# Kernel tuning notes

Measured on AMD Instinct MI355X. Metric: run time of the kernel, lower is better.

The kernel has to match this reference:

```python
import jax, jax.numpy as jnp
import numpy as np

# Model dims (match init_kwargs)
D_MODEL = 512
NUM_EXPERTS = 8
TOP_K = 2
FFN_MULT = 2
HIDDEN = FFN_MULT * D_MODEL
BATCH, SEQ = 4, 2048


def setup_inputs() -> dict:
    key = jax.random.key(0)
    k_x, k_g, k_bg, k_w1, k_w3, k_w2 = jax.random.split(key, 6)
    sd = 1.0 / np.sqrt(D_MODEL).astype(np.float32)
    sh = 1.0 / np.sqrt(HIDDEN).astype(np.float32)
    return {
        "x": jax.random.normal(k_x, (BATCH, SEQ, D_MODEL), dtype=jnp.float32),
        # gate: nn.Linear(d_model, num_experts) with bias
        "Wg": jax.random.normal(k_g, (D_MODEL, NUM_EXPERTS), dtype=jnp.float32) * sd,
        "bg": jax.random.normal(k_bg, (NUM_EXPERTS,), dtype=jnp.float32) * 0.01,
        # stacked per-expert SwiGLU FFN params (no bias, LLaMA-style)
        "W1": jax.random.normal(k_w1, (NUM_EXPERTS, D_MODEL, HIDDEN), dtype=jnp.float32) * sd,
        "W3": jax.random.normal(k_w3, (NUM_EXPERTS, D_MODEL, HIDDEN), dtype=jnp.float32) * sd,
        "W2": jax.random.normal(k_w2, (NUM_EXPERTS, HIDDEN, D_MODEL), dtype=jnp.float32) * sh,
    }


def reference(x, Wg, bg, W1, W3, W2):
    B, S, D = x.shape
    E = Wg.shape[1]
    xt = x.reshape(-1, D)                        # [T, D], T = B*S
    T = xt.shape[0]

    # Router: top-k over experts, softmax over the k selected logits
    logits = xt @ Wg + bg                        # [T, E]
    top_vals, top_idx = jax.lax.top_k(logits, TOP_K)  # [T, K]
    top_probs = jax.nn.softmax(top_vals, axis=-1)     # [T, K]

    # Dense per-(token, expert) combine weight; zero where expert not selected.
    # top-k indices are distinct per token so scatter-add == scatter-set.
    gate_w = jnp.zeros((T, E), dtype=xt.dtype).at[
        jnp.arange(T)[:, None], top_idx
    ].add(top_probs)                              # [T, E]

    # Loop over experts (fixed, small), accumulate weighted expert outputs.
    def body(y, expert):
        w1, w3, w2, g = expert                   # g: [T]
        h = jax.nn.silu(xt @ w1) * (xt @ w3)     # [T, H]
        return y + g[:, None] * (h @ w2), None

    y0 = jnp.zeros_like(xt)
    y, _ = jax.lax.scan(body, y0, (W1, W3, W2, gate_w.T))
    return y.reshape(B, S, D)
```

## Files before the change

kernel.cpp:

```cpp
#include <hip/hip_runtime.h>
#include <hip/hip_bf16.h>

#define TOKENS 8192
#define DM 512
#define NE 8
#define HID 1024
#define NSLOT (TOKENS * 2)
#define NB 32

#define BM 128
#define BN 64
#define BK 64
#define MAXTILE 136

typedef __bf16 bf16x8 __attribute__((ext_vector_type(8)));
typedef float floatx4 __attribute__((ext_vector_type(4)));
typedef unsigned short u16x8 __attribute__((ext_vector_type(8)));

__device__ __forceinline__ unsigned short f2bf(float f) {
    union { float f; unsigned u; } c; c.f = f;
    unsigned u = c.u;
    u += 0x7fffu + ((u >> 16) & 1u);
    return (unsigned short)(u >> 16);
}

__device__ __forceinline__ void load16_lds(const void* g, void* l) {
    __builtin_amdgcn_global_load_lds(
        (const __attribute__((address_space(1))) unsigned int*)g,
        (__attribute__((address_space(3))) unsigned int*)l, 16, 0, 0);
}

__global__ void cvt_transpose_kernel(const float* __restrict__ W1, const float* __restrict__ W3,
                                     const float* __restrict__ W2,
                                     unsigned short* __restrict__ w1t, unsigned short* __restrict__ w3t,
                                     unsigned short* __restrict__ w2t) {
    __shared__ float tile[32][33];
    const float* src; unsigned short* dst; int K, N;
    if (blockIdx.y == 0)      { src = W1; dst = w1t; K = DM;  N = HID; }
    else if (blockIdx.y == 1) { src = W3; dst = w3t; K = DM;  N = HID; }
    else                      { src = W2; dst = w2t; K = HID; N = DM;  }
    const int tk = K >> 5, tn = N >> 5;
    int b = blockIdx.x;
    int e = b / (tk * tn);
    int rem = b % (tk * tn);
    int kt = rem / tn, nt = rem % tn;
    int tx = threadIdx.x & 31, ty = threadIdx.x >> 5;
    const float* s = src + ((size_t)e * K + kt * 32) * N + nt * 32;
    #pragma unroll
    for (int i = 0; i < 32; i += 8)
        tile[ty + i][tx] = s[(size_t)(ty + i) * N + tx];
    __syncthreads();
    unsigned short* d = dst + ((size_t)e * N + nt * 32) * K + kt * 32;
    #pragma unroll
    for (int i = 0; i < 32; i += 8)
        d[(size_t)(ty + i) * K + tx] = f2bf(tile[tx][ty + i]);
}

__global__ void router_kernel(const float* __restrict__ x, const float* __restrict__ Wg,
                              const float* __restrict__ bg,
                              int* __restrict__ top_idx, float* __restrict__ top_p,
                              unsigned short* __restrict__ xb) {
    int lane = threadIdx.x & 63, wave = threadIdx.x >> 6;
    int t = blockIdx.x * 4 + wave;
    float acc[NE];
    #pragma unroll
    for (int e = 0; e < NE; e++) acc[e] = 0.f;
    const float* xr = x + (size_t)t * DM;
    unsigned short* xbr = xb + (size_t)t * DM;
    #pragma unroll
    for (int j = 0; j < 8; j++) {
        int d = lane + j * 64;
        float xv = xr[d];
        xbr[d] = f2bf(xv);
        const float4* wr = (const float4*)(Wg + (size_t)d * NE);
        float4 w0 = wr[0], w1 = wr[1];
        acc[0] += xv * w0.x; acc[1] += xv * w0.y; acc[2] += xv * w0.z; acc[3] += xv * w0.w;
        acc[4] += xv * w1.x; acc[5] += xv * w1.y; acc[6] += xv * w1.z; acc[7] += xv * w1.w;
    }
    #pragma unroll
    for (int e = 0; e < NE; e++) {
        float v = acc[e];
        #pragma unroll
        for (int off = 32; off > 0; off >>= 1) v += __shfl_down(v, off, 64);
        acc[e] = v;
    }
    if (lane == 0) {
        float best = -1e30f, second = -1e30f;
        int bi = 0, si = 0;
        #pragma unroll
        for (int e = 0; e < NE; e++) {
            float v = acc[e] + bg[e];
            if (v > best) { second = best; si = bi; best = v; bi = e; }
            else if (v > second) { second = v; si = e; }
        }
        float ex = __expf(second - best);
        float inv = 1.f / (1.f + ex);
        top_idx[t * 2] = bi;  top_idx[t * 2 + 1] = si;
        top_p[t * 2] = inv;   top_p[t * 2 + 1] = ex * inv;
    }
}

__global__ void hist_kernel(const int* __restrict__ top_idx, int* __restrict__ block_hist) {
    __shared__ int h[NE];
    int b = blockIdx.x, tid = threadIdx.x;
    if (tid < NE) h[tid] = 0;
    __syncthreads();
    int t = b * 256 + tid;
    atomicAdd(&h[top_idx[t * 2]], 1);
    atomicAdd(&h[top_idx[t * 2 + 1]], 1);
    __syncthreads();
    if (tid < NE) block_hist[b * NE + tid] = h[tid];
}

__global__ void prefix_kernel(const int* __restrict__ block_hist, int* __restrict__ counts,
                              int* __restrict__ offsets, int* __restrict__ bases) {
    int e = threadIdx.x;
    if (e < NE) {
        int run = 0;
        for (int b = 0; b < NB; b++) { bases[b * NE + e] = run; run += block_hist[b * NE + e]; }
        counts[e] = run;
    }
    __syncthreads();
    if (e == 0) {
        int s = 0;
        for (int ee = 0; ee < NE; ee++) { offsets[ee] = s; s += counts[ee]; }
    }
    __syncthreads();
    if (e < NE) {
        int off = offsets[e];
        for (int b = 0; b < NB; b++) bases[b * NE + e] += off;
    }
}

__global__ void build_kernel(const int* __restrict__ top_idx, const float* __restrict__ top_p,
                             const int* __restrict__ bases,
                             int* __restrict__ rows, float* __restrict__ gates,
                             int* __restrict__ slot_of) {
    __shared__ int cur[NE];
    int b = blockIdx.x, tid = threadIdx.x;
    if (tid < NE) cur[tid] = bases[b * NE + tid];
    __syncthreads();
    int t = b * 256 + tid;
    #pragma unroll
    for (int k = 0; k < 2; k++) {
        int e = top_idx[t * 2 + k];
        int slot = atomicAdd(&cur[e], 1);
        rows[slot] = t;
        gates[slot] = top_p[t * 2 + k];
        slot_of[t * 2 + k] = slot;
    }
}

__device__ __forceinline__ bool tile_lookup(const int* counts, const int* offsets, int gy,
                                            int& e, int& mt, int& cnt, int& off) {
    int bacc = 0;
    #pragma unroll
    for (int ee = 0; ee < NE; ee++) {
        int c = counts[ee];
        int ntl = (c + BM - 1) >> 7;
        if (gy < bacc + ntl) { e = ee; mt = gy - bacc; cnt = c; off = offsets[ee]; return true; }
        bacc += ntl;
    }
    return false;
}

__global__ __launch_bounds__(256) void gemm1_kernel(
    const unsigned short* __restrict__ xb,
    const unsigned short* __restrict__ w1t,
    const unsigned short* __restrict__ w3t,
    unsigned short* __restrict__ Hb,
    const int* __restrict__ rows, const int* __restrict__ counts,
    const int* __restrict__ offsets) {
    const int nt = blockIdx.x;
    int e, mt, cnt, off;
    if (!tile_lookup(counts, offsets, blockIdx.y, e, mt, cnt, off)) return;

    __shared__ unsigned short As[2][BM * BK];
    __shared__ unsigned short B1s[2][BN * BK];
    __shared__ unsigned short B3s[2][BN * BK];

    const int tid = threadIdx.x;
    const int lane = tid & 63, wave = tid >> 6;
    const int lrow8 = lane >> 3;
    const int lchunk = (lane & 7) ^ lrow8;

    const unsigned short* a_g[4];
    #pragma unroll
    for (int i = 0; i < 4; i++) {
        int r = (wave * 4 + i) * 8 + lrow8;
        int gr = mt * BM + r;
        int tok = rows[off + (gr < cnt ? gr : 0)];
        a_g[i] = xb + (size_t)tok * DM + lchunk * 8;
    }
    const unsigned short* b1_g[2]; const unsigned short* b3_g[2];
    #pragma unroll
    for (int i = 0; i < 2; i++) {
        int r = (wave * 2 + i) * 8 + lrow8;
        b1_g[i] = w1t + ((size_t)e * HID + nt * BN + r) * DM + lchunk * 8;
        b3_g[i] = w3t + ((size_t)e * HID + nt * BN + r) * DM + lchunk * 8;
    }

    const int l15 = lane & 15, quad = lane >> 4;
    const int sw = l15 & 7;

    floatx4 acc1[2][4], acc3[2][4];
    #pragma unroll
    for (int i = 0; i < 2; i++)
        #pragma unroll
        for (int j = 0; j < 4; j++) {
            acc1[i][j] = (floatx4){0.f, 0.f, 0.f, 0.f};
            acc3[i][j] = (floatx4){0.f, 0.f, 0.f, 0.f};
        }

    auto stage = [&](int k0, int b) {
        #pragma unroll
        for (int i = 0; i < 4; i++) load16_lds(a_g[i] + k0, &As[b][(wave * 4 + i) * 512]);
        #pragma unroll
        for (int i = 0; i < 2; i++) {
            load16_lds(b1_g[i] + k0, &B1s[b][(wave * 2 + i) * 512]);
            load16_lds(b3_g[i] + k0, &B3s[b][(wave * 2 + i) * 512]);
        }
    };
    auto compute = [&](int b) {
        #pragma unroll
        for (int kk = 0; kk < 2; kk++) {
            const int qc = kk * 4 + quad;
            const int ch = (qc ^ sw) << 3;
            bf16x8 af[2], b1f[4], b3f[4];
            #pragma unroll
            for (int mi = 0; mi < 2; mi++)
                af[mi] = *(const bf16x8*)(&As[b][(wave * 32 + mi * 16 + l15) * 64 + ch]);
            #pragma unroll
            for (int ni = 0; ni < 4; ni++) {
                b1f[ni] = *(const bf16x8*)(&B1s[b][(ni * 16 + l15) * 64 + ch]);
                b3f[ni] = *(const bf16x8*)(&B3s[b][(ni * 16 + l15) * 64 + ch]);
            }
            #pragma unroll
            for (int mi = 0; mi < 2; mi++)
                #pragma unroll
                for (int ni = 0; ni < 4; ni++) {
                    acc1[mi][ni] = __builtin_amdgcn_mfma_f32_16x16x32_bf16(af[mi], b1f[ni], acc1[mi][ni], 0, 0, 0);
                    acc3[mi][ni] = __builtin_amdgcn_mfma_f32_16x16x32_bf16(af[mi], b3f[ni], acc3[mi][ni], 0, 0, 0);
                }
        }
    };

    const int NI = DM / BK;
    stage(0, 0);
    #pragma unroll
    for (int i = 0; i < NI; i += 2) {
        __syncthreads();
        if (i + 1 < NI) stage((i + 1) * BK, 1);
        compute(0);
        __syncthreads();
        if (i + 2 < NI) stage((i + 2) * BK, 0);
        compute(1);
    }
    #pragma unroll
    for (int mi = 0; mi < 2; mi++) {
        #pragma unroll
        for (int r = 0; r < 4; r++) {
            int mloc = wave * 32 + mi * 16 + quad * 4 + r;
            int gi = mt * BM + mloc;
            if (gi < cnt) {
                size_t rowbase = (size_t)(off + gi) * HID + nt * BN;
                #pragma unroll
                for (int ni = 0; ni < 4; ni++) {
                    float z1 = acc1[mi][ni][r];
                    float z3 = acc3[mi][ni][r];
                    float h = (z1 / (1.f + __expf(-z1))) * z3;
                    Hb[rowbase + ni * 16 + l15] = f2bf(h);
                }
            }
        }
    }
}

__global__ __launch_bounds__(256) void gemm2_kernel(
    const unsigned short* __restrict__ Hb,
    const unsigned short* __restrict__ w2t,
    unsigned short* __restrict__ P,
    const float* __restrict__ gates,
    const int* __restrict__ counts, const int* __restrict__ offsets) {
    const int nt = blockIdx.x;
    int e, mt, cnt, off;
    if (!tile_lookup(counts, offsets, blockIdx.y, e, mt, cnt, off)) return;

    __shared__ unsigned short As[2][BM * BK];
    __shared__ unsigned short Bs[2][BN * BK];

    const int tid = threadIdx.x;
    const int lane = tid & 63, wave = tid >> 6;
    const int lrow8 = lane >> 3;
    const int lchunk = (lane & 7) ^ lrow8;

    const unsigned short* a_g[4];
    #pragma unroll
    for (int i = 0; i < 4; i++) {
        int r = (wave * 4 + i) * 8 + lrow8;
        int sl = off + mt * BM + r;
        if (sl >= NSLOT) sl = NSLOT - 1;
        a_g[i] = Hb + (size_t)sl * HID + lchunk * 8;
    }
    const unsigned short* b_g[2];
    #pragma unroll
    for (int i = 0; i < 2; i++) {
        int r = (wave * 2 + i) * 8 + lrow8;
        b_g[i] = w2t + ((size_t)e * DM + nt * BN + r) * HID + lchunk * 8;
    }

    const int l15 = lane & 15, quad = lane >> 4;
    const int sw = l15 & 7;

    floatx4 acc[2][4];
    #pragma unroll
    for (int i = 0; i < 2; i++)
        #pragma unroll
        for (int j = 0; j < 4; j++) acc[i][j] = (floatx4){0.f, 0.f, 0.f, 0.f};

    auto stage = [&](int k0, int b) {
        #pragma unroll
        for (int i = 0; i < 4; i++) load16_lds(a_g[i] + k0, &As[b][(wave * 4 + i) * 512]);
        #pragma unroll
        for (int i = 0; i < 2; i++) load16_lds(b_g[i] + k0, &Bs[b][(wave * 2 + i) * 512]);
    };
    auto compute = [&](int b) {
        #pragma unroll
        for (int kk = 0; kk < 2; kk++) {
            const int qc = kk * 4 + quad;
            const int ch = (qc ^ sw) << 3;
            bf16x8 af[2], bf[4];
            #pragma unroll
            for (int mi = 0; mi < 2; mi++)
                af[mi] = *(const bf16x8*)(&As[b][(wave * 32 + mi * 16 + l15) * 64 + ch]);
            #pragma unroll
            for (int ni = 0; ni < 4; ni++)
                bf[ni] = *(const bf16x8*)(&Bs[b][(ni * 16 + l15) * 64 + ch]);
            #pragma unroll
            for (int mi = 0; mi < 2; mi++)
                #pragma unroll
                for (int ni = 0; ni < 4; ni++)
                    acc[mi][ni] = __builtin_amdgcn_mfma_f32_16x16x32_bf16(af[mi], bf[ni], acc[mi][ni], 0, 0, 0);
        }
    };

    const int NI = HID / BK;
    stage(0, 0);
    #pragma unroll
    for (int i = 0; i < NI; i += 2) {
        __syncthreads();
        if (i + 1 < NI) stage((i + 1) * BK, 1);
        compute(0);
        __syncthreads();
        if (i + 2 < NI) stage((i + 2) * BK, 0);
        compute(1);
    }
    #pragma unroll
    for (int mi = 0; mi < 2; mi++) {
        #pragma unroll
        for (int r = 0; r < 4; r++) {
            int mloc = wave * 32 + mi * 16 + quad * 4 + r;
            int gi = mt * BM + mloc;
            if (gi < cnt) {
                int slot = off + gi;
                float g = gates[slot];
                #pragma unroll
                for (int ni = 0; ni < 4; ni++) {
                    int col = nt * BN + ni * 16 + l15;
                    P[(size_t)slot * DM + col] = f2bf(g * acc[mi][ni][r]);
                }
            }
        }
    }
}

__global__ void combine_kernel(const unsigned short* __restrict__ P,
                               const int* __restrict__ slot_of, float* __restrict__ y) {
    int i = blockIdx.x * blockDim.x + threadIdx.x;
    int t = i / (DM / 8);
    int c8 = i % (DM / 8);
    int s0 = slot_of[t * 2], s1 = slot_of[t * 2 + 1];
    uint4 a = *(const uint4*)(P + (size_t)s0 * DM + c8 * 8);
    uint4 b = *(const uint4*)(P + (size_t)s1 * DM + c8 * 8);
    float o[8];
    const unsigned* aw = (const unsigned*)&a;
    const unsigned* bw = (const unsigned*)&b;
    #pragma unroll
    for (int j = 0; j < 4; j++) {
        union { unsigned u; float f; } al, ah, bl, bh;
        al.u = aw[j] << 16; ah.u = aw[j] & 0xffff0000u;
        bl.u = bw[j] << 16; bh.u = bw[j] & 0xffff0000u;
        o[j * 2]     = al.f + bl.f;
        o[j * 2 + 1] = ah.f + bh.f;
    }
    float4* yo = (float4*)(y + (size_t)t * DM + c8 * 8);
    yo[0] = make_float4(o[0], o[1], o[2], o[3]);
    yo[1] = make_float4(o[4], o[5], o[6], o[7]);
}

extern "C" void kernel_launch(void* const* d_in, const int* in_sizes, int n_in,
                              void* d_out, int out_size, void* d_ws, size_t ws_size,
                              hipStream_t stream) {
    (void)in_sizes; (void)n_in; (void)out_size; (void)ws_size;
    const float* x  = (const float*)d_in[0];
    const float* Wg = (const float*)d_in[1];
    const float* bg = (const float*)d_in[2];
    const float* W1 = (const float*)d_in[3];
    const float* W3 = (const float*)d_in[4];
    const float* W2 = (const float*)d_in[5];
    float* y = (float*)d_out;

    char* p = (char*)d_ws;
    auto carve = [&](size_t bytes) -> char* {
        char* r = p;
        p += (bytes + 255) & ~(size_t)255;
        return r;
    };
    unsigned short* xb   = (unsigned short*)carve((size_t)TOKENS * DM * 2);
    unsigned short* w1t  = (unsigned short*)carve((size_t)NE * DM * HID * 2);
    unsigned short* w3t  = (unsigned short*)carve((size_t)NE * DM * HID * 2);
    unsigned short* w2t  = (unsigned short*)carve((size_t)NE * HID * DM * 2);
    unsigned short* Hb   = (unsigned short*)carve((size_t)NSLOT * HID * 2);
    int*   rows    = (int*)carve(NSLOT * 4);
    float* gates   = (float*)carve(NSLOT * 4);
    int*   slot_of = (int*)carve(NSLOT * 4);
    int*   tidx    = (int*)carve((size_t)TOKENS * 2 * 4);
    float* tp      = (float*)carve((size_t)TOKENS * 2 * 4);
    int*   counts  = (int*)carve(256);
    int*   offsets = (int*)carve(256);
    int*   bhist   = (int*)carve((size_t)NB * NE * 4);
    int*   bases   = (int*)carve((size_t)NB * NE * 4);
    unsigned short* P = w1t;

    router_kernel<<<dim3(TOKENS / 4), dim3(256), 0, stream>>>(x, Wg, bg, tidx, tp, xb);
    cvt_transpose_kernel<<<dim3(NE * 16 * 32, 3), dim3(256), 0, stream>>>(W1, W3, W2, w1t, w3t, w2t);
    hist_kernel<<<dim3(NB), dim3(256), 0, stream>>>(tidx, bhist);
    prefix_kernel<<<dim3(1), dim3(64), 0, stream>>>(bhist, counts, offsets, bases);
    build_kernel<<<dim3(NB), dim3(256), 0, stream>>>(tidx, tp, bases, rows, gates, slot_of);
    gemm1_kernel<<<dim3(HID / BN, MAXTILE), dim3(256), 0, stream>>>(xb, w1t, w3t, Hb, rows, counts, offsets);
    gemm2_kernel<<<dim3(DM / BN, MAXTILE), dim3(256), 0, stream>>>(Hb, w2t, P, gates, counts, offsets);
    combine_kernel<<<dim3((TOKENS * DM / 8) / 256), dim3(256), 0, stream>>>(P, slot_of, y);
}
```

Measured before the change: 232.2 us.

## Vectorize weight transpose-convert and remap GEMM blocks for XCD-local L2 reuse

Result: faster. 216.3 us (-6.8%).

```diff
diff --git a/kernel.cpp b/kernel.cpp
--- a/kernel.cpp
+++ b/kernel.cpp
@@ -34,26 +34,37 @@
                                      const float* __restrict__ W2,
                                      unsigned short* __restrict__ w1t, unsigned short* __restrict__ w3t,
                                      unsigned short* __restrict__ w2t) {
-    __shared__ float tile[32][33];
+    __shared__ float tile[64][65];
     const float* src; unsigned short* dst; int K, N;
     if (blockIdx.y == 0)      { src = W1; dst = w1t; K = DM;  N = HID; }
     else if (blockIdx.y == 1) { src = W3; dst = w3t; K = DM;  N = HID; }
     else                      { src = W2; dst = w2t; K = HID; N = DM;  }
-    const int tk = K >> 5, tn = N >> 5;
+    const int tkn = (K >> 6) * (N >> 6);
     int b = blockIdx.x;
-    int e = b / (tk * tn);
-    int rem = b % (tk * tn);
-    int kt = rem / tn, nt = rem % tn;
-    int tx = threadIdx.x & 31, ty = threadIdx.x >> 5;
-    const float* s = src + ((size_t)e * K + kt * 32) * N + nt * 32;
-    #pragma unroll
-    for (int i = 0; i < 32; i += 8)
-        tile[ty + i][tx] = s[(size_t)(ty + i) * N + tx];
-    __syncthreads();
-    unsigned short* d = dst + ((size_t)e * N + nt * 32) * K + kt * 32;
-    #pragma unroll
-    for (int i = 0; i < 32; i += 8)
-        d[(size_t)(ty + i) * K + tx] = f2bf(tile[tx][ty + i]);
+    int e = b / tkn;
+    int rem = b % tkn;
+    const int tn6 = N >> 6;
+    int kt = rem / tn6, nt = rem % tn6;
+    int tx = threadIdx.x & 15, ty = threadIdx.x >> 4;
+    const float* s = src + ((size_t)(e * K + kt * 64 + ty)) * N + nt * 64 + tx * 4;
+    #pragma unroll
+    for (int i = 0; i < 4; i++) {
+        float4 v = *(const float4*)(s + (size_t)(i * 16) * N);
+        float* tr = &tile[ty + i * 16][tx * 4];
+        tr[0] = v.x; tr[1] = v.y; tr[2] = v.z; tr[3] = v.w;
+    }
+    __syncthreads();
+    int n = threadIdx.x >> 3;
+    int c8 = (threadIdx.x & 7) * 8;
+    unsigned short* d = dst + ((size_t)(e * N + nt * 64)) * K + kt * 64;
+    #pragma unroll
+    for (int i = 0; i < 2; i++) {
+        int nn = n + i * 32;
+        u16x8 r;
+        #pragma unroll
+        for (int kk = 0; kk < 8; kk++) r[kk] = f2bf(tile[c8 + kk][nn]);
+        *(u16x8*)(d + (size_t)nn * K + c8) = r;
+    }
 }
 
 __global__ void router_kernel(const float* __restrict__ x, const float* __restrict__ Wg,
@@ -171,9 +182,13 @@
     unsigned short* __restrict__ Hb,
     const int* __restrict__ rows, const int* __restrict__ counts,
     const int* __restrict__ offsets) {
-    const int nt = blockIdx.x;
+    const int lid = blockIdx.x;
+    const int xcd = lid & 7;
+    const int j = lid >> 3;
+    const int gy = xcd * (MAXTILE / 8) + (j >> 4);
+    const int nt = j & 15;
     int e, mt, cnt, off;
-    if (!tile_lookup(counts, offsets, blockIdx.y, e, mt, cnt, off)) return;
+    if (!tile_lookup(counts, offsets, gy, e, mt, cnt, off)) return;
 
     __shared__ unsigned short As[2][BM * BK];
     __shared__ unsigned short B1s[2][BN * BK];
@@ -207,9 +222,9 @@
     #pragma unroll
     for (int i = 0; i < 2; i++)
         #pragma unroll
-        for (int j = 0; j < 4; j++) {
-            acc1[i][j] = (floatx4){0.f, 0.f, 0.f, 0.f};
-            acc3[i][j] = (floatx4){0.f, 0.f, 0.f, 0.f};
+        for (int j2 = 0; j2 < 4; j2++) {
+            acc1[i][j2] = (floatx4){0.f, 0.f, 0.f, 0.f};
+            acc3[i][j2] = (floatx4){0.f, 0.f, 0.f, 0.f};
         }
 
     auto stage = [&](int k0, int b) {
@@ -282,9 +297,13 @@
     unsigned short* __restrict__ P,
     const float* __restrict__ gates,
     const int* __restrict__ counts, const int* __restrict__ offsets) {
-    const int nt = blockIdx.x;
+    const int lid = blockIdx.x;
+    const int xcd = lid & 7;
+    const int j = lid >> 3;
+    const int gy = xcd * (MAXTILE / 8) + (j >> 3);
+    const int nt = j & 7;
     int e, mt, cnt, off;
-    if (!tile_lookup(counts, offsets, blockIdx.y, e, mt, cnt, off)) return;
+    if (!tile_lookup(counts, offsets, gy, e, mt, cnt, off)) return;
 
     __shared__ unsigned short As[2][BM * BK];
     __shared__ unsigned short Bs[2][BN * BK];
@@ -316,7 +335,7 @@
     #pragma unroll
     for (int i = 0; i < 2; i++)
         #pragma unroll
-        for (int j = 0; j < 4; j++) acc[i][j] = (floatx4){0.f, 0.f, 0.f, 0.f};
+        for (int j2 = 0; j2 < 4; j2++) acc[i][j2] = (floatx4){0.f, 0.f, 0.f, 0.f};
 
     auto stage = [&](int k0, int b) {
         #pragma unroll
@@ -433,11 +452,11 @@
     unsigned short* P = w1t;
 
     router_kernel<<<dim3(TOKENS / 4), dim3(256), 0, stream>>>(x, Wg, bg, tidx, tp, xb);
-    cvt_transpose_kernel<<<dim3(NE * 16 * 32, 3), dim3(256), 0, stream>>>(W1, W3, W2, w1t, w3t, w2t);
+    cvt_transpose_kernel<<<dim3(NE * 8 * 16, 3), dim3(256), 0, stream>>>(W1, W3, W2, w1t, w3t, w2t);
     hist_kernel<<<dim3(NB), dim3(256), 0, stream>>>(tidx, bhist);
     prefix_kernel<<<dim3(1), dim3(64), 0, stream>>>(bhist, counts, offsets, bases);
     build_kernel<<<dim3(NB), dim3(256), 0, stream>>>(tidx, tp, bases, rows, gates, slot_of);
-    gemm1_kernel<<<dim3(HID / BN, MAXTILE), dim3(256), 0, stream>>>(xb, w1t, w3t, Hb, rows, counts, offsets);
-    gemm2_kernel<<<dim3(DM / BN, MAXTILE), dim3(256), 0, stream>>>(Hb, w2t, P, gates, counts, offsets);
+    gemm1_kernel<<<dim3((HID / BN) * MAXTILE), dim3(256), 0, stream>>>(xb, w1t, w3t, Hb, rows, counts, offsets);
+    gemm2_kernel<<<dim3((DM / BN) * MAXTILE), dim3(256), 0, stream>>>(Hb, w2t, P, gates, counts, offsets);
     combine_kernel<<<dim3((TOKENS * DM / 8) / 256), dim3(256), 0, stream>>>(P, slot_of, y);
 }
```
